# Optimization experiments

Measured on AMD Instinct MI355X. Metric: run time of the kernel, lower is better.

Reference implementation:

```python
import jax, jax.numpy as jnp
import numpy as np

HIDDEN = 1024
N_HEAD = 16
HEAD_DIM = HIDDEN // N_HEAD


def setup_inputs() -> dict:
    key = jax.random.key(0)
    ks = jax.random.split(key, 11)
    B, S, D, H, E = 4, 1024, HIDDEN, N_HEAD, HEAD_DIM
    sc = 0.02
    return {
        "query": jax.random.normal(ks[0], (B, S, D), jnp.float32),
        "key": jax.random.normal(ks[1], (B, S, D), jnp.float32),
        "value": jax.random.normal(ks[2], (B, S, D), jnp.float32),
        # per-head projection weights stacked over heads (torch Linear: y = x @ W.T + b)
        "Wq": jax.random.normal(ks[3], (H, D, E), jnp.float32) * sc,
        "bq": jax.random.normal(ks[4], (H, E), jnp.float32) * sc,
        "Wk": jax.random.normal(ks[5], (H, D, E), jnp.float32) * sc,
        "bk": jax.random.normal(ks[6], (H, E), jnp.float32) * sc,
        "Wv": jax.random.normal(ks[7], (H, D, E), jnp.float32) * sc,
        "bv": jax.random.normal(ks[8], (H, E), jnp.float32) * sc,
        "Wo": jax.random.normal(ks[9], (D, D), jnp.float32) * sc,
        "bo": jax.random.normal(ks[10], (D,), jnp.float32) * sc,
    }


def reference(query, key, value, Wq, bq, Wk, bk, Wv, bv, Wo, bo):
    B, S, D = query.shape
    H, _, E = Wq.shape
    # per-head linear projections (vectorized over heads)
    q = jnp.einsum("bsd,hde->bhse", query, Wq) + bq[None, :, None, :]
    k = jnp.einsum("bsd,hde->bhse", key, Wk) + bk[None, :, None, :]
    v = jnp.einsum("bsd,hde->bhse", value, Wv) + bv[None, :, None, :]
    scale = jnp.sqrt(jnp.asarray(E, q.dtype))
    scores = jnp.einsum("bhse,bhte->bhst", q, k) / scale  # [B,H,S,S]
    attn = jax.nn.softmax(scores, axis=-1)  # dropout is identity in eval
    wv = jnp.einsum("bhst,bhte->bhse", attn, v)  # [B,H,S,E]
    # concat heads along feature dim (head h -> slice h*E:(h+1)*E)
    wv = wv.transpose(0, 2, 1, 3).reshape(B, S, H * E)
    out = wv @ Wo.T + bo  # final linear; output dropout identity in eval
    return out
```

## Files before the change

### kernel.cpp

```cpp
#include <hip/hip_runtime.h>

typedef unsigned short u16;
typedef __attribute__((ext_vector_type(8))) short bf16x8;
typedef __attribute__((ext_vector_type(4))) float f32x4;

#define B_SZ 4
#define S_SZ 1024
#define D_SZ 1024
#define H_SZ 16
#define E_SZ 64
#define M_SZ (B_SZ * S_SZ)

__device__ __forceinline__ u16 f2bf(float f) {
  union { float f; unsigned u; } x; x.f = f;
  unsigned r = (x.u + 0x7FFFu + ((x.u >> 16) & 1u)) >> 16;
  return (u16)r;
}

__device__ __forceinline__ void async16(const void* g, void* l) {
  __builtin_amdgcn_global_load_lds(
      (const __attribute__((address_space(1))) void*)g,
      (__attribute__((address_space(3))) void*)l, 16, 0, 0);
}

__device__ __forceinline__ f32x4 mfma16(bf16x8 a, bf16x8 b, f32x4 c) {
  return __builtin_amdgcn_mfma_f32_16x16x32_bf16(a, b, c, 0, 0, 0);
}

__global__ void cast3(const float* __restrict__ q, const float* __restrict__ k,
                      const float* __restrict__ v, u16* __restrict__ oq,
                      u16* __restrict__ ok, u16* __restrict__ ov) {
  int gid = blockIdx.x * 256 + threadIdx.x;
  int sel = gid >> 19;
  int i = (gid & ((1 << 19) - 1)) << 3;
  const float* in = sel == 0 ? q : (sel == 1 ? k : v);
  u16* out = sel == 0 ? oq : (sel == 1 ? ok : ov);
  float4 a = *(const float4*)(in + i);
  float4 b = *(const float4*)(in + i + 4);
  alignas(16) u16 r[8];
  r[0] = f2bf(a.x); r[1] = f2bf(a.y); r[2] = f2bf(a.z); r[3] = f2bf(a.w);
  r[4] = f2bf(b.x); r[5] = f2bf(b.y); r[6] = f2bf(b.z); r[7] = f2bf(b.w);
  *(uint4*)(out + i) = *(uint4*)r;
}

__global__ void cast_bf16_k(const float* __restrict__ in, u16* __restrict__ out, int n) {
  int i = (blockIdx.x * 256 + threadIdx.x) * 8;
  if (i >= n) return;
  float4 a = *(const float4*)(in + i);
  float4 b = *(const float4*)(in + i + 4);
  alignas(16) u16 r[8];
  r[0] = f2bf(a.x); r[1] = f2bf(a.y); r[2] = f2bf(a.z); r[3] = f2bf(a.w);
  r[4] = f2bf(b.x); r[5] = f2bf(b.y); r[6] = f2bf(b.z); r[7] = f2bf(b.w);
  *(uint4*)(out + i) = *(uint4*)r;
}

__global__ void transW3(const float* __restrict__ Wq, const float* __restrict__ Wk,
                        const float* __restrict__ Wv, u16* __restrict__ Tq,
                        u16* __restrict__ Tk, u16* __restrict__ Tv) {
  __shared__ float tile[64 * 68];
  const int wsel = blockIdx.x >> 8;
  const int bi = blockIdx.x & 255;
  const float* W = wsel == 0 ? Wq : (wsel == 1 ? Wk : Wv);
  u16* WT = wsel == 0 ? Tq : (wsel == 1 ? Tk : Tv);
  const int tid = threadIdx.x;
  const int h = bi >> 4;
  const int d0 = (bi & 15) << 6;
#pragma unroll
  for (int c = 0; c < 4; ++c) {
    const int dd = c * 16 + (tid >> 4);
    const int e4 = (tid & 15) << 2;
    float4 vq = *(const float4*)(W + (h << 16) + ((d0 + dd) << 6) + e4);
    *(float4*)(tile + dd * 68 + e4) = vq;
  }
  __syncthreads();
  {
    const int e = tid >> 2;
    const int dc = (tid & 3) << 4;
    alignas(16) u16 outv[16];
#pragma unroll
    for (int i = 0; i < 16; ++i) outv[i] = f2bf(tile[(dc + i) * 68 + e]);
    u16* dst = WT + (((size_t)(h << 6) + e) << 10) + d0 + dc;
    *(uint4*)(dst) = *(uint4*)outv;
    *(uint4*)(dst + 8) = *(uint4*)(outv + 8);
  }
}

__device__ __forceinline__ void gemm_core(const u16* __restrict__ A,
                                          const u16* __restrict__ BT,
                                          const float* __restrict__ bias,
                                          void* __restrict__ Cout,
                                          float scale, int mode, int bi) {
  __shared__ u16 Al[128 * 64];
  __shared__ u16 Bl[128 * 64];
  const int tid = threadIdx.x;
  const int wave = tid >> 6;
  const int lane = tid & 63;
  const int l15 = lane & 15, lq = lane >> 4;
  const int bm = bi >> 3;
  const int bn = bi & 7;
  const int row0 = bm << 7, col0 = bn << 7;
  const int wr = ((wave >> 1) & 1) << 6;
  const int wc = (wave & 1) << 6;

  f32x4 acc[4][4];
#pragma unroll
  for (int m = 0; m < 4; ++m)
#pragma unroll
    for (int n = 0; n < 4; ++n) acc[m][n] = (f32x4)0.0f;

  for (int k0 = 0; k0 < 1024; k0 += 64) {
    __syncthreads();
#pragma unroll
    for (int c = 0; c < 4; ++c) {
      const int x = c * 4096 + tid * 16;
      const int g = x ^ (((x >> 7) & 7) << 4);
      const int row = g >> 7;
      const int cb = g & 127;
      const u16* ga = A + (size_t)(row0 + row) * 1024 + k0 + (cb >> 1);
      const u16* gb = BT + (size_t)(col0 + row) * 1024 + k0 + (cb >> 1);
      async16(ga, (char*)Al + c * 4096 + (wave << 10));
      async16(gb, (char*)Bl + c * 4096 + (wave << 10));
    }
    __syncthreads();

    bf16x8 af[4][2], bfr[4][2];
#pragma unroll
    for (int m = 0; m < 4; ++m)
#pragma unroll
      for (int kf = 0; kf < 2; ++kf) {
        int r = wr + m * 16 + l15;
        int byte = ((r << 7) + kf * 64 + lq * 16) ^ ((r & 7) << 4);
        af[m][kf] = *(const bf16x8*)((const char*)Al + byte);
      }
#pragma unroll
    for (int n = 0; n < 4; ++n)
#pragma unroll
      for (int kf = 0; kf < 2; ++kf) {
        int r = wc + n * 16 + l15;
        int byte = ((r << 7) + kf * 64 + lq * 16) ^ ((r & 7) << 4);
        bfr[n][kf] = *(const bf16x8*)((const char*)Bl + byte);
      }
#pragma unroll
    for (int kf = 0; kf < 2; ++kf)
#pragma unroll
      for (int m = 0; m < 4; ++m)
#pragma unroll
        for (int n = 0; n < 4; ++n)
          acc[m][n] = mfma16(af[m][kf], bfr[n][kf], acc[m][n]);
  }

#pragma unroll
  for (int m = 0; m < 4; ++m)
#pragma unroll
    for (int n = 0; n < 4; ++n) {
      int col = col0 + wc + n * 16 + l15;
      float bv = bias[col];
      int rowb = row0 + wr + m * 16 + lq * 4;
      if (mode == 2) {
        alignas(8) u16 r4[4];
#pragma unroll
        for (int j = 0; j < 4; ++j) r4[j] = f2bf((acc[m][n][j] + bv) * scale);
        *(uint2*)((u16*)Cout + (size_t)col * 4096 + rowb) = *(uint2*)r4;
      } else if (mode == 1) {
#pragma unroll
        for (int j = 0; j < 4; ++j)
          ((u16*)Cout)[(size_t)(rowb + j) * 1024 + col] = f2bf((acc[m][n][j] + bv) * scale);
      } else {
#pragma unroll
        for (int j = 0; j < 4; ++j)
          ((float*)Cout)[(size_t)(rowb + j) * 1024 + col] = (acc[m][n][j] + bv) * scale;
      }
    }
}

__global__ __launch_bounds__(256)
void gemm3(const u16* __restrict__ qb, const u16* __restrict__ kb, const u16* __restrict__ vb,
           const u16* __restrict__ Tq, const u16* __restrict__ Tk, const u16* __restrict__ Tv,
           const float* __restrict__ bq, const float* __restrict__ bk, const float* __restrict__ bv,
           u16* __restrict__ Qp, u16* __restrict__ Kp, u16* __restrict__ VpT) {
  const int g = blockIdx.x >> 8;
  const int bi = blockIdx.x & 255;
  const u16* A = g == 0 ? qb : (g == 1 ? kb : vb);
  const u16* BT = g == 0 ? Tq : (g == 1 ? Tk : Tv);
  const float* bias = g == 0 ? bq : (g == 1 ? bk : bv);
  void* out = g == 0 ? (void*)Qp : (g == 1 ? (void*)Kp : (void*)VpT);
  gemm_core(A, BT, bias, out, g == 0 ? 0.125f : 1.0f, g == 2 ? 2 : 1, bi);
}

__global__ __launch_bounds__(256)
void gemmO(const u16* __restrict__ A, const u16* __restrict__ BT,
           const float* __restrict__ bias, float* __restrict__ out) {
  gemm_core(A, BT, bias, out, 1.0f, 0, blockIdx.x);
}

__global__ __launch_bounds__(256)
void attn(const u16* __restrict__ Qp, const u16* __restrict__ Kp,
          const u16* __restrict__ VpT, u16* __restrict__ Ow) {
  __shared__ alignas(16) u16 Kl[2][64 * 64];
  __shared__ alignas(16) u16 VTl[2][64 * 64];
  __shared__ alignas(16) u16 Pl[4][16 * 64];
  const int tid = threadIdx.x;
  const int wave = tid >> 6;
  const int lane = tid & 63;
  const int l15 = lane & 15, lq = lane >> 4;
  const int qt = blockIdx.x & 15;
  const int bh = blockIdx.x >> 4;
  const int b = bh >> 4, h = bh & 15;
  const size_t bS = (size_t)b * S_SZ;

  const int xs0 = tid * 16, xs1 = 4096 + tid * 16;
  const int r0 = xs0 >> 7, r1 = xs1 >> 7;
  const int c0 = ((xs0 & 127) ^ (((xs0 >> 7) & 7) << 4)) >> 1;
  const int c1 = ((xs1 & 127) ^ (((xs1 >> 7) & 7) << 4)) >> 1;
  const u16* Kb0 = Kp + ((bS + r0) << 10) + h * 64 + c0;
  const u16* Kb1 = Kp + ((bS + r1) << 10) + h * 64 + c1;
  const u16* Vb0 = VpT + (size_t)(h * 64 + r0) * 4096 + bS + c0;
  const u16* Vb1 = VpT + (size_t)(h * 64 + r1) * 4096 + bS + c1;

  bf16x8 aq[2];
  {
    const u16* qptr = Qp + ((bS + qt * 64 + wave * 16 + l15) << 10) + h * 64 + lq * 8;
    aq[0] = *(const bf16x8*)(qptr);
    aq[1] = *(const bf16x8*)(qptr + 32);
  }

  f32x4 o[4];
#pragma unroll
  for (int n = 0; n < 4; ++n) o[n] = (f32x4)0.0f;
  float m_run[4] = {-1e30f, -1e30f, -1e30f, -1e30f};
  float l_run[4] = {0.f, 0.f, 0.f, 0.f};
  u16* Pw = Pl[wave];

  async16(Kb0, (char*)Kl[0] + xs0);
  async16(Kb1, (char*)Kl[0] + xs1);
  async16(Vb0, (char*)VTl[0] + xs0);
  async16(Vb1, (char*)VTl[0] + xs1);
  __syncthreads();

  int buf = 0;
  for (int t0 = 0; t0 < S_SZ; t0 += 64) {
    if (t0 + 64 < S_SZ) {
      const int tn = t0 + 64;
      async16(Kb0 + ((size_t)tn << 10), (char*)Kl[buf ^ 1] + xs0);
      async16(Kb1 + ((size_t)tn << 10), (char*)Kl[buf ^ 1] + xs1);
      async16(Vb0 + tn, (char*)VTl[buf ^ 1] + xs0);
      async16(Vb1 + tn, (char*)VTl[buf ^ 1] + xs1);
    }

    f32x4 s[4];
#pragma unroll
    for (int n = 0; n < 4; ++n) s[n] = (f32x4)0.0f;
#pragma unroll
    for (int n = 0; n < 4; ++n)
#pragma unroll
      for (int kf = 0; kf < 2; ++kf) {
        int r = n * 16 + l15;
        int byte = ((r << 7) + kf * 64 + lq * 16) ^ ((r & 7) << 4);
        bf16x8 bk = *(const bf16x8*)((const char*)Kl[buf] + byte);
        s[n] = mfma16(aq[kf], bk, s[n]);
      }

    float mx[4], alpha[4], rs[4];
#pragma unroll
    for (int j = 0; j < 4; ++j)
      mx[j] = fmaxf(fmaxf(s[0][j], s[1][j]), fmaxf(s[2][j], s[3][j]));
#pragma unroll
    for (int off = 1; off < 16; off <<= 1)
#pragma unroll
      for (int j = 0; j < 4; ++j)
        mx[j] = fmaxf(mx[j], __shfl_xor(mx[j], off, 64));
#pragma unroll
    for (int j = 0; j < 4; ++j) {
      float mn = fmaxf(m_run[j], mx[j]);
      alpha[j] = __expf(m_run[j] - mn);
      m_run[j] = mn;
      rs[j] = 0.f;
    }
#pragma unroll
    for (int n = 0; n < 4; ++n)
#pragma unroll
      for (int j = 0; j < 4; ++j) {
        float p = __expf(s[n][j] - m_run[j]);
        rs[j] += p;
        int row = lq * 4 + j;
        int t = n * 16 + l15;
        int byte = (row << 7) + ((t << 1) ^ ((row & 7) << 4));
        *(u16*)((char*)Pw + byte) = f2bf(p);
      }
#pragma unroll
    for (int off = 1; off < 16; off <<= 1)
#pragma unroll
      for (int j = 0; j < 4; ++j)
        rs[j] += __shfl_xor(rs[j], off, 64);
#pragma unroll
    for (int j = 0; j < 4; ++j) l_run[j] = l_run[j] * alpha[j] + rs[j];
#pragma unroll
    for (int n = 0; n < 4; ++n)
#pragma unroll
      for (int j = 0; j < 4; ++j) o[n][j] *= alpha[j];

#pragma unroll
    for (int kf = 0; kf < 2; ++kf) {
      int pbyte = (l15 << 7) + ((kf * 64 + lq * 16) ^ ((l15 & 7) << 4));
      bf16x8 pa = *(const bf16x8*)((const char*)Pw + pbyte);
#pragma unroll
      for (int n = 0; n < 4; ++n) {
        int vr = n * 16 + l15;
        int byte = ((vr << 7) + kf * 64 + lq * 16) ^ ((vr & 7) << 4);
        bf16x8 bv = *(const bf16x8*)((const char*)VTl[buf] + byte);
        o[n] = mfma16(pa, bv, o[n]);
      }
    }

    __syncthreads();
    buf ^= 1;
  }

#pragma unroll
  for (int n = 0; n < 4; ++n)
#pragma unroll
    for (int j = 0; j < 4; ++j) {
      float val = o[n][j] / l_run[j];
      int row = qt * 64 + wave * 16 + lq * 4 + j;
      int col = h * 64 + n * 16 + l15;
      Ow[((bS + row) << 10) + col] = f2bf(val);
    }
}

extern "C" void kernel_launch(void* const* d_in, const int* in_sizes, int n_in,
                              void* d_out, int out_size, void* d_ws, size_t ws_size,
                              hipStream_t stream) {
  const float* q  = (const float*)d_in[0];
  const float* k  = (const float*)d_in[1];
  const float* v  = (const float*)d_in[2];
  const float* Wq = (const float*)d_in[3];
  const float* bq = (const float*)d_in[4];
  const float* Wk = (const float*)d_in[5];
  const float* bk = (const float*)d_in[6];
  const float* Wv = (const float*)d_in[7];
  const float* bv = (const float*)d_in[8];
  const float* Wo = (const float*)d_in[9];
  const float* bo = (const float*)d_in[10];

  char* w = (char*)d_ws;
  const size_t MB = 1u << 20;
  u16* qb  = (u16*)(w + 0 * MB);
  u16* kb  = (u16*)(w + 8 * MB);
  u16* vb  = (u16*)(w + 16 * MB);
  u16* WqT = (u16*)(w + 24 * MB);
  u16* WkT = (u16*)(w + 26 * MB);
  u16* WvT = (u16*)(w + 28 * MB);
  u16* Wob = (u16*)(w + 30 * MB);
  u16* Qp  = (u16*)(w + 32 * MB);
  u16* Kp  = (u16*)(w + 40 * MB);
  u16* VpT = (u16*)(w + 48 * MB);
  u16* wvb = (u16*)(w + 56 * MB);

  const int nW = H_SZ * D_SZ * E_SZ;

  cast3<<<6144, 256, 0, stream>>>(q, k, v, qb, kb, vb);
  cast_bf16_k<<<nW / 2048, 256, 0, stream>>>(Wo, Wob, nW);
  transW3<<<768, 256, 0, stream>>>(Wq, Wk, Wv, WqT, WkT, WvT);

  gemm3<<<768, 256, 0, stream>>>(qb, kb, vb, WqT, WkT, WvT, bq, bk, bv, Qp, Kp, VpT);

  attn<<<B_SZ * H_SZ * (S_SZ / 64), 256, 0, stream>>>(Qp, Kp, VpT, wvb);

  gemmO<<<256, 256, 0, stream>>>(wvb, Wob, bo, (float*)d_out);
}
```

Before: 150.5 us.

## Transpose QK^T MFMA so each lane owns one query row and defer softmax rescaling

Swaps the MFMA operand order so the score tile is transposed and each lane holds scores for a single query row. Row max and sum then need only two cross-lane shuffles instead of a 4x4 butterfly, and P is written to LDS as packed 8-byte stores instead of scattered 2-byte stores. It also adds a lazy rescale: the running max and the output rescale update only when some row's max grows by more than 8, which skips exp/multiply work on most tiles. The risk is larger unnormalized exponent values, which must stay within fp32 and bf16 range, plus extra shuffles to redistribute alpha and l per row.

```diff
diff --git a/kernel.cpp b/kernel.cpp
--- a/kernel.cpp
+++ b/kernel.cpp
@@ -1,6 +1,7 @@
 #include <hip/hip_runtime.h>
 
 typedef unsigned short u16;
+typedef unsigned int u32;
 typedef __attribute__((ext_vector_type(8))) short bf16x8;
 typedef __attribute__((ext_vector_type(4))) float f32x4;
 
@@ -15,6 +16,10 @@
   union { float f; unsigned u; } x; x.f = f;
   unsigned r = (x.u + 0x7FFFu + ((x.u >> 16) & 1u)) >> 16;
   return (u16)r;
+}
+
+__device__ __forceinline__ u32 pack_bf16(float lo, float hi) {
+  return (u32)f2bf(lo) | ((u32)f2bf(hi) << 16);
 }
 
 __device__ __forceinline__ void async16(const void* g, void* l) {
@@ -227,8 +232,8 @@
   f32x4 o[4];
 #pragma unroll
   for (int n = 0; n < 4; ++n) o[n] = (f32x4)0.0f;
-  float m_run[4] = {-1e30f, -1e30f, -1e30f, -1e30f};
-  float l_run[4] = {0.f, 0.f, 0.f, 0.f};
+  float m_run = -1e30f;
+  float l_run = 0.f;
   u16* Pw = Pl[wave];
 
   async16(Kb0, (char*)Kl[0] + xs0);
@@ -257,47 +262,49 @@
         int r = n * 16 + l15;
         int byte = ((r << 7) + kf * 64 + lq * 16) ^ ((r & 7) << 4);
         bf16x8 bk = *(const bf16x8*)((const char*)Kl[buf] + byte);
-        s[n] = mfma16(aq[kf], bk, s[n]);
-      }
-
-    float mx[4], alpha[4], rs[4];
-#pragma unroll
-    for (int j = 0; j < 4; ++j)
-      mx[j] = fmaxf(fmaxf(s[0][j], s[1][j]), fmaxf(s[2][j], s[3][j]));
-#pragma unroll
-    for (int off = 1; off < 16; off <<= 1)
-#pragma unroll
-      for (int j = 0; j < 4; ++j)
-        mx[j] = fmaxf(mx[j], __shfl_xor(mx[j], off, 64));
-#pragma unroll
-    for (int j = 0; j < 4; ++j) {
-      float mn = fmaxf(m_run[j], mx[j]);
-      alpha[j] = __expf(m_run[j] - mn);
-      m_run[j] = mn;
-      rs[j] = 0.f;
-    }
+        s[n] = mfma16(bk, aq[kf], s[n]);
+      }
+
+    float mx = s[0][0];
 #pragma unroll
     for (int n = 0; n < 4; ++n)
 #pragma unroll
-      for (int j = 0; j < 4; ++j) {
-        float p = __expf(s[n][j] - m_run[j]);
-        rs[j] += p;
-        int row = lq * 4 + j;
-        int t = n * 16 + l15;
-        int byte = (row << 7) + ((t << 1) ^ ((row & 7) << 4));
-        *(u16*)((char*)Pw + byte) = f2bf(p);
-      }
-#pragma unroll
-    for (int off = 1; off < 16; off <<= 1)
-#pragma unroll
-      for (int j = 0; j < 4; ++j)
-        rs[j] += __shfl_xor(rs[j], off, 64);
-#pragma unroll
-    for (int j = 0; j < 4; ++j) l_run[j] = l_run[j] * alpha[j] + rs[j];
-#pragma unroll
-    for (int n = 0; n < 4; ++n)
-#pragma unroll
-      for (int j = 0; j < 4; ++j) o[n][j] *= alpha[j];
+      for (int j = 0; j < 4; ++j) mx = fmaxf(mx, s[n][j]);
+    mx = fmaxf(mx, __shfl_xor(mx, 16, 64));
+    mx = fmaxf(mx, __shfl_xor(mx, 32, 64));
+
+    if (__any(mx > m_run + 8.0f)) {
+      float mn = fmaxf(m_run, mx);
+      float alpha = __expf(m_run - mn);
+      m_run = mn;
+      l_run *= alpha;
+      float a0 = __shfl(alpha, lq * 4 + 0, 64);
+      float a1 = __shfl(alpha, lq * 4 + 1, 64);
+      float a2 = __shfl(alpha, lq * 4 + 2, 64);
+      float a3 = __shfl(alpha, lq * 4 + 3, 64);
+#pragma unroll
+      for (int n = 0; n < 4; ++n) {
+        o[n][0] *= a0; o[n][1] *= a1; o[n][2] *= a2; o[n][3] *= a3;
+      }
+    }
+
+    float rs = 0.f;
+#pragma unroll
+    for (int n = 0; n < 4; ++n) {
+      float p0 = __expf(s[n][0] - m_run);
+      float p1 = __expf(s[n][1] - m_run);
+      float p2 = __expf(s[n][2] - m_run);
+      float p3 = __expf(s[n][3] - m_run);
+      rs += (p0 + p1) + (p2 + p3);
+      u32 lo = pack_bf16(p0, p1);
+      u32 hi = pack_bf16(p2, p3);
+      int byte = (l15 << 7) + (((n * 32 + lq * 8)) ^ ((l15 & 7) << 4));
+      uint2 wv; wv.x = lo; wv.y = hi;
+      *(uint2*)((char*)Pw + byte) = wv;
+    }
+    rs += __shfl_xor(rs, 16, 64);
+    rs += __shfl_xor(rs, 32, 64);
+    l_run += rs;
 
 #pragma unroll
     for (int kf = 0; kf < 2; ++kf) {
@@ -316,15 +323,21 @@
     buf ^= 1;
   }
 
-#pragma unroll
-  for (int n = 0; n < 4; ++n)
+  float li0 = __shfl(l_run, lq * 4 + 0, 64);
+  float li1 = __shfl(l_run, lq * 4 + 1, 64);
+  float li2 = __shfl(l_run, lq * 4 + 2, 64);
+  float li3 = __shfl(l_run, lq * 4 + 3, 64);
+  float inv0 = 1.0f / li0, inv1 = 1.0f / li1, inv2 = 1.0f / li2, inv3 = 1.0f / li3;
+#pragma unroll
+  for (int n = 0; n < 4; ++n) {
+    float vals[4] = {o[n][0] * inv0, o[n][1] * inv1, o[n][2] * inv2, o[n][3] * inv3};
 #pragma unroll
     for (int j = 0; j < 4; ++j) {
-      float val = o[n][j] / l_run[j];
       int row = qt * 64 + wave * 16 + lq * 4 + j;
       int col = h * 64 + n * 16 + l15;
-      Ow[((bS + row) << 10) + col] = f2bf(val);
-    }
+      Ow[((bS + row) << 10) + col] = f2bf(vals[j]);
+    }
+  }
 }
 
 extern "C" void kernel_launch(void* const* d_in, const int* in_sizes, int n_in,
```

After: 134.0 us. 1.12x faster.
